# Kernel optimization log

Measured on AMD Instinct MI355X. Metric: run time of the kernel, lower is better.

Reference implementation:

```python
import jax, jax.numpy as jnp
import numpy as np
import math

B, SES, SEQ, H, K = 16, 16, 64, 512, 32
L = SES * SEQ


def setup_inputs() -> dict:
    key = jax.random.key(0)
    ks = jax.random.split(key, 16)
    s = 1.0 / math.sqrt(H)
    return {
        "user_emb": jax.random.normal(ks[0], (B, H), jnp.float32),
        "item_emb": jax.random.normal(ks[1], (B, SES, SEQ, H), jnp.float32),
        "mask": jnp.zeros((B, L, K), jnp.float32),
        "index": jax.random.randint(ks[2], (L, K), 0, L, jnp.int64),
        "Wq": jax.random.normal(ks[3], (H, H), jnp.float32) * s,
        "bq": jnp.zeros((H,), jnp.float32),
        "Wk": jax.random.normal(ks[4], (H, H), jnp.float32) * s,
        "bk": jnp.zeros((H,), jnp.float32),
        "Wv": jax.random.normal(ks[5], (H, H), jnp.float32) * s,
        "bv": jnp.zeros((H,), jnp.float32),
        "Wd": jax.random.normal(ks[6], (H, H), jnp.float32) * s,
        "bd": jnp.zeros((H,), jnp.float32),
        "ln_g": jnp.ones((H,), jnp.float32),
        "ln_b": jnp.zeros((H,), jnp.float32),
    }


def reference(user_emb, item_emb, mask, index, Wq, bq, Wk, bk, Wv, bv, Wd, bd, ln_g, ln_b):
    b, ses, seq, h = item_emb.shape
    l = ses * seq
    item_flat = item_emb.reshape(b, l, h)
    q = user_emb @ Wq.T + bq                       # [B, H]
    k = item_flat @ Wk.T + bk                      # [B, L, H]
    v = item_flat @ Wv.T + bv                      # [B, L, H]
    # scalar query against all L keys, scaled by sqrt(hidden_size)
    scores = jnp.einsum("bh,blh->bl", q, k) / math.sqrt(h)
    scores = scores[:, index] + mask               # gather -> [B, L, K]
    w = jax.nn.softmax(scores, axis=-1)            # [B, L, K]
    vg = v[:, index, :]                            # gather -> [B, L, K, H]
    attn_out = jnp.einsum("blk,blkh->blh", w, vg)  # [B, L, H]
    dense = attn_out @ Wd.T + bd
    x = dense + item_flat                          # residual (dropout = identity, eval)
    mu = jnp.mean(x, axis=-1, keepdims=True)
    var = jnp.var(x, axis=-1, keepdims=True)
    y = (x - mu) / jnp.sqrt(var + 1e-12) * ln_g + ln_b
    return y.reshape(b, ses, seq, h)
```

## Files before the change

### kernel.cpp

```cpp
#include <hip/hip_runtime.h>
#include <math.h>

constexpr int HD   = 512;
constexpr int LL   = 1024;
constexpr int MT   = 16384;
constexpr int KNBR = 32;
constexpr float SCL = 0.04419417382415922f;

typedef __attribute__((ext_vector_type(8))) short  bf16x8;
typedef __attribute__((ext_vector_type(4))) float  f32x4;

__device__ inline float b2f(unsigned short u) {
    union { unsigned int i; float f; } v; v.i = (unsigned int)u << 16; return v.f;
}
__device__ inline float b2f_lo(unsigned int u) {
    union { unsigned int i; float f; } v; v.i = u << 16; return v.f;
}
__device__ inline float b2f_hi(unsigned int u) {
    union { unsigned int i; float f; } v; v.i = u & 0xffff0000u; return v.f;
}
__device__ inline unsigned short f2b(float x) {
    union { float f; unsigned int u; } v; v.f = x;
    unsigned int r = v.u + 0x7fff + ((v.u >> 16) & 1);
    return (unsigned short)(r >> 16);
}

constexpr int PB_CONV_I = 8192;
constexpr int PB_CONV_W = 512;
constexpr int PB_Q      = 2048;

__global__ __launch_bounds__(256) void prep(
    const float* __restrict__ item, const float* __restrict__ Wv,
    const float* __restrict__ Wd, const float* __restrict__ u,
    const float* __restrict__ Wq, const float* __restrict__ bq,
    unsigned short* __restrict__ item_bf, unsigned short* __restrict__ item_kt,
    unsigned short* __restrict__ Wv_bf, unsigned short* __restrict__ Wd_bf,
    float* __restrict__ q)
{
    const int blk = blockIdx.x, tid = threadIdx.x;

    if (blk < PB_CONV_I) {
        const int i = blk * 1024 + tid * 4;
        float4 v = *(const float4*)&item[i];
        ushort4 o;
        o.x = f2b(v.x); o.y = f2b(v.y); o.z = f2b(v.z); o.w = f2b(v.w);
        *(ushort4*)&item_bf[i] = o;
        const int m = i >> 9, k = i & 511;
        *(ushort4*)&item_kt[((size_t)(k >> 5) * MT + m) * 32 + (k & 31)] = o;
        return;
    }
    if (blk < PB_CONV_I + PB_CONV_W) {
        const int n = HD*HD;
        const int i = (blk - PB_CONV_I) * 1024 + tid * 4;
        const float* s; unsigned short* d; int off;
        if (i < n) { s = Wv; d = Wv_bf; off = i; }
        else       { s = Wd; d = Wd_bf; off = i - n; }
        float4 v = *(const float4*)&s[off];
        ushort4 o;
        o.x = f2b(v.x); o.y = f2b(v.y); o.z = f2b(v.z); o.w = f2b(v.w);
        const int nr = off >> 9, k = off & 511;
        *(ushort4*)&d[((k >> 5) * 512 + nr) * 32 + (k & 31)] = o;
        return;
    }
    {
        const int wid  = (blk - PB_CONV_I - PB_CONV_W) * 4 + (tid >> 6);
        const int lane = tid & 63;
        const int b = wid >> 9, h = wid & 511;
        const float* ur = &u[b*HD + lane*8];
        const float* wr = &Wq[(size_t)h*HD + lane*8];
        const float4 u0 = *(const float4*)ur, u1 = *(const float4*)(ur+4);
        const float4 w0 = *(const float4*)wr, w1 = *(const float4*)(wr+4);
        float acc = u0.x*w0.x + u0.y*w0.y + u0.z*w0.z + u0.w*w0.w
                  + u1.x*w1.x + u1.y*w1.y + u1.z*w1.z + u1.w*w1.w;
        #pragma unroll
        for (int off = 32; off; off >>= 1) acc += __shfl_down(acc, off);
        if (lane == 0) q[b*HD + h] = acc + bq[h];
    }
}

__global__ __launch_bounds__(256) void gemm_v_r(
    const unsigned short* __restrict__ Akt, const unsigned short* __restrict__ Wt,
    const float* __restrict__ bv, const float* __restrict__ Wk,
    const float* __restrict__ bk, const float* __restrict__ q,
    unsigned short* __restrict__ v_bf, float* __restrict__ rbuf,
    float* __restrict__ s0buf)
{
    __shared__ unsigned short As[2][128 * 32];
    __shared__ unsigned short Bs[2][128 * 32];

    const int blk = blockIdx.x;
    const int tid = threadIdx.x;

    if (blk >= 512) {
        if (blk < 640) {
            __shared__ float red[4][64];
            const int rblk = blk - 512;
            const int b = rblk >> 3, c0 = (rblk & 7) * 64;
            const int cl = tid & 63, hg = tid >> 6;
            const float* qb = &q[b*HD];
            const float* wb = &Wk[(size_t)hg*128*HD + c0 + cl];
            float acc = 0.f;
            #pragma unroll 8
            for (int h = 0; h < 128; h++)
                acc += qb[hg*128 + h] * wb[(size_t)h*HD];
            red[hg][cl] = acc;
            __syncthreads();
            if (tid < 64)
                rbuf[b*HD + c0 + tid] = SCL *
                    (red[0][tid] + red[1][tid] + red[2][tid] + red[3][tid]);
        } else {
            __shared__ float sp[4];
            const int b = blk - 640;
            float p = q[b*HD + tid]*bk[tid] + q[b*HD + tid + 256]*bk[tid + 256];
            #pragma unroll
            for (int off = 32; off; off >>= 1) p += __shfl_down(p, off);
            if ((tid & 63) == 0) sp[tid >> 6] = p;
            __syncthreads();
            if (tid == 0) s0buf[b] = (sp[0] + sp[1] + sp[2] + sp[3]) * SCL;
        }
        return;
    }

    const int rowb = (blk & 7) | ((blk >> 5) << 3);
    const int colb = (blk >> 3) & 3;
    const int row0 = rowb * 128;
    const int col0 = colb * 128;

    const int wave = tid >> 6, lane = tid & 63;
    const int wm = (wave >> 1) * 64;
    const int wn = (wave & 1)  * 64;

    const int lrr = lane >> 2;
    const int cc  = lane & 3;
    int st_row[2], st_gchunk[2];
    #pragma unroll
    for (int t = 0; t < 2; t++) {
        const int m = wave*32 + t*16 + lrr;
        st_row[t]    = m;
        st_gchunk[t] = cc ^ ((m >> 1) & 3);
    }

    const int fr   = lane & 15;
    const int quad = lane >> 4;

    f32x4 acc[4][4];
    #pragma unroll
    for (int i = 0; i < 4; i++)
        #pragma unroll
        for (int j = 0; j < 4; j++)
            acc[i][j] = (f32x4){0.f, 0.f, 0.f, 0.f};

    int a_off[4], b_off[4];
    #pragma unroll
    for (int i = 0; i < 4; i++) {
        const int m = wm + i*16 + fr;
        a_off[i] = m*32 + ((quad ^ ((m >> 1) & 3)) << 3);
        const int n = wn + i*16 + fr;
        b_off[i] = n*32 + ((quad ^ ((n >> 1) & 3)) << 3);
    }

    auto stage = [&](int bf, int kt) {
        #pragma unroll
        for (int t = 0; t < 2; t++) {
            const int m = st_row[t];
            const unsigned short* ga =
                &Akt[((size_t)kt*MT + row0 + m)*32 + st_gchunk[t]*8];
            __builtin_amdgcn_global_load_lds(
                (const __attribute__((address_space(1))) void*)ga,
                (__attribute__((address_space(3))) void*)&As[bf][(wave*32 + t*16)*32],
                16, 0, 0);
            const unsigned short* gw =
                &Wt[((size_t)kt*512 + col0 + m)*32 + st_gchunk[t]*8];
            __builtin_amdgcn_global_load_lds(
                (const __attribute__((address_space(1))) void*)gw,
                (__attribute__((address_space(3))) void*)&Bs[bf][(wave*32 + t*16)*32],
                16, 0, 0);
        }
    };

    stage(0, 0);
    stage(1, 1);

    for (int s = 0; s < 15; ++s) {
        asm volatile("s_waitcnt vmcnt(4)" ::: "memory");
        __builtin_amdgcn_s_barrier();
        asm volatile("" ::: "memory");

        const int cur = s & 1;
        bf16x8 af[4], bfr[4];
        #pragma unroll
        for (int i = 0; i < 4; i++) {
            af[i]  = *(const bf16x8*)&As[cur][a_off[i]];
            bfr[i] = *(const bf16x8*)&Bs[cur][b_off[i]];
        }
        asm volatile("s_waitcnt lgkmcnt(0)" ::: "memory");
        __builtin_amdgcn_sched_barrier(0);
        __builtin_amdgcn_s_barrier();

        if (s + 2 < 16) stage(cur, s + 2);

        __builtin_amdgcn_s_setprio(1);
        #pragma unroll
        for (int i = 0; i < 4; i++)
            #pragma unroll
            for (int j = 0; j < 4; j++)
                acc[i][j] = __builtin_amdgcn_mfma_f32_16x16x32_bf16(
                    af[i], bfr[j], acc[i][j], 0, 0, 0);
        __builtin_amdgcn_s_setprio(0);
    }
    {
        asm volatile("s_waitcnt vmcnt(0)" ::: "memory");
        __builtin_amdgcn_s_barrier();
        asm volatile("" ::: "memory");
        bf16x8 af[4], bfr[4];
        #pragma unroll
        for (int i = 0; i < 4; i++) {
            af[i]  = *(const bf16x8*)&As[1][a_off[i]];
            bfr[i] = *(const bf16x8*)&Bs[1][b_off[i]];
        }
        asm volatile("s_waitcnt lgkmcnt(0)" ::: "memory");
        __builtin_amdgcn_sched_barrier(0);
        #pragma unroll
        for (int i = 0; i < 4; i++)
            #pragma unroll
            for (int j = 0; j < 4; j++)
                acc[i][j] = __builtin_amdgcn_mfma_f32_16x16x32_bf16(
                    af[i], bfr[j], acc[i][j], 0, 0, 0);
    }

    #pragma unroll
    for (int j = 0; j < 4; j++) {
        const int col = col0 + wn + j*16 + fr;
        const float bb = bv[col];
        #pragma unroll
        for (int i = 0; i < 4; i++) {
            #pragma unroll
            for (int r = 0; r < 4; r++) {
                const int row = row0 + wm + i*16 + quad*4 + r;
                v_bf[(size_t)row*HD + col] = f2b(acc[i][j][r] + bb);
            }
        }
    }
}

__global__ __launch_bounds__(256) void gp_scores(
    const float* __restrict__ rbuf, const float* __restrict__ s0buf,
    const unsigned short* __restrict__ item_bf, float* __restrict__ scores)
{
    const int m = blockIdx.x * 4 + (threadIdx.x >> 6);
    const int lane = threadIdx.x & 63;
    const int b = m >> 10;
    const unsigned short* ir = &item_bf[(size_t)m*HD + lane*8];
    const uint4 iv = *(const uint4*)ir;
    const float* rr = &rbuf[b*HD + lane*8];
    const float4 r0 = *(const float4*)rr;
    const float4 r1 = *(const float4*)(rr + 4);
    float acc = r0.x*b2f_lo(iv.x) + r0.y*b2f_hi(iv.x)
              + r0.z*b2f_lo(iv.y) + r0.w*b2f_hi(iv.y)
              + r1.x*b2f_lo(iv.z) + r1.y*b2f_hi(iv.z)
              + r1.z*b2f_lo(iv.w) + r1.w*b2f_hi(iv.w);
    #pragma unroll
    for (int off = 32; off; off >>= 1) acc += __shfl_down(acc, off);
    if (lane == 0) scores[m] = acc + s0buf[b];
}

__global__ __launch_bounds__(256) void gp_attn(
    const float* __restrict__ scores, const int* __restrict__ index,
    const float* __restrict__ mask, const unsigned short* __restrict__ v,
    unsigned short* __restrict__ attn)
{
    const int bid = blockIdx.x;
    const int m = ((bid & 7) << 11) | ((bid >> 3) << 2) | (int)(threadIdx.x >> 6);
    const int lane = threadIdx.x & 63;
    const int b = m >> 10, l = m & 1023;

    const int t = lane & 31;
    const int idx = index[l*KNBR + t];
    const float s = scores[b*LL + idx] + mask[(size_t)m*KNBR + t];

    float mx = s;
    #pragma unroll
    for (int off = 16; off; off >>= 1) mx = fmaxf(mx, __shfl_xor(mx, off));
    const float e = __expf(s - mx);
    float sum = e;
    #pragma unroll
    for (int off = 16; off; off >>= 1) sum += __shfl_xor(sum, off);
    const float w = e / sum;

    const unsigned short* vb = v + (size_t)(b << 10) * HD;
    const int loff = lane * 8;
    float a[8] = {};
    #pragma unroll 8
    for (int t2 = 0; t2 < KNBR; t2++) {
        const int   it = __builtin_amdgcn_readlane(idx, t2);
        const float wt = __int_as_float(
            __builtin_amdgcn_readlane(__float_as_int(w), t2));
        const uint4 pv = *(const uint4*)(vb + (size_t)it*HD + loff);
        a[0] += wt * b2f_lo(pv.x); a[1] += wt * b2f_hi(pv.x);
        a[2] += wt * b2f_lo(pv.y); a[3] += wt * b2f_hi(pv.y);
        a[4] += wt * b2f_lo(pv.z); a[5] += wt * b2f_hi(pv.z);
        a[6] += wt * b2f_lo(pv.w); a[7] += wt * b2f_hi(pv.w);
    }
    uint4 o;
    o.x = (unsigned int)f2b(a[0]) | ((unsigned int)f2b(a[1]) << 16);
    o.y = (unsigned int)f2b(a[2]) | ((unsigned int)f2b(a[3]) << 16);
    o.z = (unsigned int)f2b(a[4]) | ((unsigned int)f2b(a[5]) << 16);
    o.w = (unsigned int)f2b(a[6]) | ((unsigned int)f2b(a[7]) << 16);
    *(uint4*)&attn[(size_t)m*HD + lane*8] = o;
}

__global__ __launch_bounds__(256) void dense_ln(
    const unsigned short* __restrict__ A,
    const unsigned short* __restrict__ Wt,
    const float* __restrict__ bd, const unsigned short* __restrict__ res,
    const float* __restrict__ ln_g, const float* __restrict__ ln_b,
    float* __restrict__ out)
{
    __shared__ unsigned short As[2][32 * 32];
    __shared__ unsigned short Bs[2][512 * 32];
    __shared__ float rsum[4][32], rsq[4][32];

    const int tid  = threadIdx.x;
    const int wave = tid >> 6, lane = tid & 63;
    const int row0 = blockIdx.x * 32;

    const int lrr = lane >> 2;
    const int cc  = lane & 3;
    const int fr   = lane & 15;
    const int quad = lane >> 4;

    f32x4 acc[2][8];
    #pragma unroll
    for (int i = 0; i < 2; i++)
        #pragma unroll
        for (int j = 0; j < 8; j++)
            acc[i][j] = (f32x4){0.f, 0.f, 0.f, 0.f};

    int a_off[2], b_off[8];
    #pragma unroll
    for (int i = 0; i < 2; i++) {
        const int m = i*16 + fr;
        a_off[i] = m*32 + ((quad ^ ((m >> 1) & 3)) << 3);
    }
    #pragma unroll
    for (int j = 0; j < 8; j++) {
        const int n = wave*128 + j*16 + fr;
        b_off[j] = n*32 + ((quad ^ ((n >> 1) & 3)) << 3);
    }

    auto stage = [&](int bf, int kt) {
        #pragma unroll
        for (int t = 0; t < 8; t++) {
            const int n   = wave*128 + t*16 + lrr;
            const int gch = cc ^ ((n >> 1) & 3);
            const unsigned short* gw = &Wt[((size_t)kt*512 + n)*32 + gch*8];
            __builtin_amdgcn_global_load_lds(
                (const __attribute__((address_space(1))) void*)gw,
                (__attribute__((address_space(3))) void*)&Bs[bf][(wave*128 + t*16)*32],
                16, 0, 0);
        }
        if (wave < 2) {
            const int mm  = wave*16 + lrr;
            const int gch = cc ^ ((mm >> 1) & 3);
            const unsigned short* ga = &A[(size_t)(row0 + mm)*HD + kt*32 + gch*8];
            __builtin_amdgcn_global_load_lds(
                (const __attribute__((address_space(1))) void*)ga,
                (__attribute__((address_space(3))) void*)&As[bf][(wave*16)*32],
                16, 0, 0);
        }
    };

    stage(0, 0);
    stage(1, 1);

    for (int s = 0; s < 15; ++s) {
        if (wave < 2) asm volatile("s_waitcnt vmcnt(9)" ::: "memory");
        else          asm volatile("s_waitcnt vmcnt(8)" ::: "memory");
        __builtin_amdgcn_s_barrier();
        asm volatile("" ::: "memory");

        const int cur = s & 1;
        bf16x8 af[2], bfr[8];
        #pragma unroll
        for (int i = 0; i < 2; i++) af[i] = *(const bf16x8*)&As[cur][a_off[i]];
        #pragma unroll
        for (int j = 0; j < 8; j++) bfr[j] = *(const bf16x8*)&Bs[cur][b_off[j]];
        asm volatile("s_waitcnt lgkmcnt(0)" ::: "memory");
        __builtin_amdgcn_sched_barrier(0);
        __builtin_amdgcn_s_barrier();

        if (s + 2 < 16) stage(cur, s + 2);

        __builtin_amdgcn_s_setprio(1);
        #pragma unroll
        for (int i = 0; i < 2; i++)
            #pragma unroll
            for (int j = 0; j < 8; j++)
                acc[i][j] = __builtin_amdgcn_mfma_f32_16x16x32_bf16(
                    af[i], bfr[j], acc[i][j], 0, 0, 0);
        __builtin_amdgcn_s_setprio(0);
    }
    {
        asm volatile("s_waitcnt vmcnt(0)" ::: "memory");
        __builtin_amdgcn_s_barrier();
        asm volatile("" ::: "memory");
        bf16x8 af[2], bfr[8];
        #pragma unroll
        for (int i = 0; i < 2; i++) af[i] = *(const bf16x8*)&As[1][a_off[i]];
        #pragma unroll
        for (int j = 0; j < 8; j++) bfr[j] = *(const bf16x8*)&Bs[1][b_off[j]];
        asm volatile("s_waitcnt lgkmcnt(0)" ::: "memory");
        __builtin_amdgcn_sched_barrier(0);
        #pragma unroll
        for (int i = 0; i < 2; i++)
            #pragma unroll
            for (int j = 0; j < 8; j++)
                acc[i][j] = __builtin_amdgcn_mfma_f32_16x16x32_bf16(
                    af[i], bfr[j], acc[i][j], 0, 0, 0);
    }
    __syncthreads();

    unsigned short* rs = (unsigned short*)Bs;
    #pragma unroll
    for (int u = 0; u < 8; u++) {
        const int id = tid*8 + u;
        const int rr = id >> 6, c8 = id & 63;
        *(uint4*)&rs[rr*528 + c8*8] =
            *(const uint4*)&res[(size_t)(row0 + rr)*HD + c8*8];
    }
    __syncthreads();

    float bdv[8], gv[8], lbv[8];
    #pragma unroll
    for (int j = 0; j < 8; j++) {
        const int col = wave*128 + j*16 + fr;
        bdv[j] = bd[col]; gv[j] = ln_g[col]; lbv[j] = ln_b[col];
    }

    #pragma unroll
    for (int i = 0; i < 2; i++) {
        #pragma unroll
        for (int r = 0; r < 4; r++) {
            const int lrow = i*16 + quad*4 + r;
            float a1 = 0.f, a2 = 0.f;
            #pragma unroll
            for (int j = 0; j < 8; j++) {
                const int col = wave*128 + j*16 + fr;
                float val = acc[i][j][r] + bdv[j] + b2f(rs[lrow*528 + col]);
                acc[i][j][r] = val;
                a1 += val; a2 += val*val;
            }
            #pragma unroll
            for (int off = 1; off < 16; off <<= 1) {
                a1 += __shfl_xor(a1, off);
                a2 += __shfl_xor(a2, off);
            }
            if (fr == 0) { rsum[wave][lrow] = a1; rsq[wave][lrow] = a2; }
        }
    }
    __syncthreads();

    #pragma unroll
    for (int i = 0; i < 2; i++) {
        #pragma unroll
        for (int r = 0; r < 4; r++) {
            const int lrow = i*16 + quad*4 + r;
            const float tot  = rsum[0][lrow] + rsum[1][lrow] + rsum[2][lrow] + rsum[3][lrow];
            const float tot2 = rsq[0][lrow]  + rsq[1][lrow]  + rsq[2][lrow]  + rsq[3][lrow];
            const float mu  = tot * (1.f/HD);
            const float var = tot2 * (1.f/HD) - mu*mu;
            const float inv = rsqrtf(var + 1e-12f);
            const size_t gr = (size_t)(row0 + lrow) * HD;
            #pragma unroll
            for (int j = 0; j < 8; j++) {
                const int col = wave*128 + j*16 + fr;
                out[gr + col] = (acc[i][j][r] - mu)*inv*gv[j] + lbv[j];
            }
        }
    }
}

extern "C" void kernel_launch(void* const* d_in, const int* in_sizes, int n_in,
                              void* d_out, int out_size, void* d_ws, size_t ws_size,
                              hipStream_t stream) {
    const float* user_emb = (const float*)d_in[0];
    const float* item_emb = (const float*)d_in[1];
    const float* mask     = (const float*)d_in[2];
    const int*   index    = (const int*)  d_in[3];
    const float* Wq = (const float*)d_in[4];  const float* bq = (const float*)d_in[5];
    const float* Wk = (const float*)d_in[6];  const float* bk = (const float*)d_in[7];
    const float* Wv = (const float*)d_in[8];  const float* bv = (const float*)d_in[9];
    const float* Wd = (const float*)d_in[10]; const float* bd = (const float*)d_in[11];
    const float* ln_g = (const float*)d_in[12];
    const float* ln_b = (const float*)d_in[13];

    float* out = (float*)d_out;

    char* p = (char*)d_ws;
    unsigned short* item_bf = (unsigned short*)p; p += (size_t)MT*HD*2;
    unsigned short* item_kt = (unsigned short*)p; p += (size_t)MT*HD*2;
    unsigned short* v_bf    = (unsigned short*)p; p += (size_t)MT*HD*2;
    unsigned short* attn_bf = (unsigned short*)p; p += (size_t)MT*HD*2;
    unsigned short* Wv_bf   = (unsigned short*)p; p += (size_t)HD*HD*2;
    unsigned short* Wd_bf   = (unsigned short*)p; p += (size_t)HD*HD*2;
    float* q      = (float*)p; p += 16*HD*4;
    float* rbuf   = (float*)p; p += 16*HD*4;
    float* s0buf  = (float*)p; p += 16*4;
    float* scores = (float*)p; p += MT*4;

    prep<<<PB_CONV_I + PB_CONV_W + PB_Q, 256, 0, stream>>>(
        item_emb, Wv, Wd, user_emb, Wq, bq,
        item_bf, item_kt, Wv_bf, Wd_bf, q);

    gemm_v_r<<<656, 256, 0, stream>>>(item_kt, Wv_bf, bv, Wk, bk, q,
                                      v_bf, rbuf, s0buf);

    gp_scores<<<MT/4, 256, 0, stream>>>(rbuf, s0buf, item_bf, scores);

    gp_attn<<<MT/4, 256, 0, stream>>>(scores, index, mask, v_bf, attn_bf);

    dense_ln<<<MT/32, 256, 0, stream>>>(attn_bf, Wd_bf, bd, item_bf,
                                        ln_g, ln_b, out);
}
```

Measured before the change: 178.5 us.

## Fuse neighbour attention into dense+LayerNorm kernel and deepen V-GEMM pipeline

```diff
diff --git a/kernel.cpp b/kernel.cpp
--- a/kernel.cpp
+++ b/kernel.cpp
@@ -85,8 +85,8 @@
     unsigned short* __restrict__ v_bf, float* __restrict__ rbuf,
     float* __restrict__ s0buf)
 {
-    __shared__ unsigned short As[2][128 * 32];
-    __shared__ unsigned short Bs[2][128 * 32];
+    __shared__ unsigned short As[4][128 * 32];
+    __shared__ unsigned short Bs[4][128 * 32];
 
     const int blk = blockIdx.x;
     const int tid = threadIdx.x;
@@ -159,7 +159,8 @@
         b_off[i] = n*32 + ((quad ^ ((n >> 1) & 3)) << 3);
     }
 
-    auto stage = [&](int bf, int kt) {
+    auto stage = [&](int kt) {
+        const int bf = kt & 3;
         #pragma unroll
         for (int t = 0; t < 2; t++) {
             const int m = st_row[t];
@@ -178,15 +179,9 @@
         }
     };
 
-    stage(0, 0);
-    stage(1, 1);
-
-    for (int s = 0; s < 15; ++s) {
-        asm volatile("s_waitcnt vmcnt(4)" ::: "memory");
+    auto kstep = [&](int cur, int kt_next) {
         __builtin_amdgcn_s_barrier();
         asm volatile("" ::: "memory");
-
-        const int cur = s & 1;
         bf16x8 af[4], bfr[4];
         #pragma unroll
         for (int i = 0; i < 4; i++) {
@@ -196,9 +191,7 @@
         asm volatile("s_waitcnt lgkmcnt(0)" ::: "memory");
         __builtin_amdgcn_sched_barrier(0);
         __builtin_amdgcn_s_barrier();
-
-        if (s + 2 < 16) stage(cur, s + 2);
-
+        if (kt_next >= 0) stage(kt_next);
         __builtin_amdgcn_s_setprio(1);
         #pragma unroll
         for (int i = 0; i < 4; i++)
@@ -207,26 +200,17 @@
                 acc[i][j] = __builtin_amdgcn_mfma_f32_16x16x32_bf16(
                     af[i], bfr[j], acc[i][j], 0, 0, 0);
         __builtin_amdgcn_s_setprio(0);
-    }
-    {
-        asm volatile("s_waitcnt vmcnt(0)" ::: "memory");
-        __builtin_amdgcn_s_barrier();
-        asm volatile("" ::: "memory");
-        bf16x8 af[4], bfr[4];
-        #pragma unroll
-        for (int i = 0; i < 4; i++) {
-            af[i]  = *(const bf16x8*)&As[1][a_off[i]];
-            bfr[i] = *(const bf16x8*)&Bs[1][b_off[i]];
-        }
-        asm volatile("s_waitcnt lgkmcnt(0)" ::: "memory");
-        __builtin_amdgcn_sched_barrier(0);
-        #pragma unroll
-        for (int i = 0; i < 4; i++)
-            #pragma unroll
-            for (int j = 0; j < 4; j++)
-                acc[i][j] = __builtin_amdgcn_mfma_f32_16x16x32_bf16(
-                    af[i], bfr[j], acc[i][j], 0, 0, 0);
-    }
+    };
+
+    stage(0); stage(1); stage(2); stage(3);
+
+    for (int s = 0; s <= 12; ++s) {
+        asm volatile("s_waitcnt vmcnt(12)" ::: "memory");
+        kstep(s & 3, (s + 4 <= 15) ? s + 4 : -1);
+    }
+    asm volatile("s_waitcnt vmcnt(8)" ::: "memory");  kstep(1, -1);
+    asm volatile("s_waitcnt vmcnt(4)" ::: "memory");  kstep(2, -1);
+    asm volatile("s_waitcnt vmcnt(0)" ::: "memory");  kstep(3, -1);
 
     #pragma unroll
     for (int j = 0; j < 4; j++) {
@@ -264,133 +248,124 @@
     if (lane == 0) scores[m] = acc + s0buf[b];
 }
 
-__global__ __launch_bounds__(256) void gp_attn(
+__global__ __launch_bounds__(512) void dense_attn_ln(
     const float* __restrict__ scores, const int* __restrict__ index,
     const float* __restrict__ mask, const unsigned short* __restrict__ v,
-    unsigned short* __restrict__ attn)
-{
-    const int bid = blockIdx.x;
-    const int m = ((bid & 7) << 11) | ((bid >> 3) << 2) | (int)(threadIdx.x >> 6);
-    const int lane = threadIdx.x & 63;
-    const int b = m >> 10, l = m & 1023;
-
-    const int t = lane & 31;
-    const int idx = index[l*KNBR + t];
-    const float s = scores[b*LL + idx] + mask[(size_t)m*KNBR + t];
-
-    float mx = s;
-    #pragma unroll
-    for (int off = 16; off; off >>= 1) mx = fmaxf(mx, __shfl_xor(mx, off));
-    const float e = __expf(s - mx);
-    float sum = e;
-    #pragma unroll
-    for (int off = 16; off; off >>= 1) sum += __shfl_xor(sum, off);
-    const float w = e / sum;
-
-    const unsigned short* vb = v + (size_t)(b << 10) * HD;
-    const int loff = lane * 8;
-    float a[8] = {};
-    #pragma unroll 8
-    for (int t2 = 0; t2 < KNBR; t2++) {
-        const int   it = __builtin_amdgcn_readlane(idx, t2);
-        const float wt = __int_as_float(
-            __builtin_amdgcn_readlane(__float_as_int(w), t2));
-        const uint4 pv = *(const uint4*)(vb + (size_t)it*HD + loff);
-        a[0] += wt * b2f_lo(pv.x); a[1] += wt * b2f_hi(pv.x);
-        a[2] += wt * b2f_lo(pv.y); a[3] += wt * b2f_hi(pv.y);
-        a[4] += wt * b2f_lo(pv.z); a[5] += wt * b2f_hi(pv.z);
-        a[6] += wt * b2f_lo(pv.w); a[7] += wt * b2f_hi(pv.w);
-    }
-    uint4 o;
-    o.x = (unsigned int)f2b(a[0]) | ((unsigned int)f2b(a[1]) << 16);
-    o.y = (unsigned int)f2b(a[2]) | ((unsigned int)f2b(a[3]) << 16);
-    o.z = (unsigned int)f2b(a[4]) | ((unsigned int)f2b(a[5]) << 16);
-    o.w = (unsigned int)f2b(a[6]) | ((unsigned int)f2b(a[7]) << 16);
-    *(uint4*)&attn[(size_t)m*HD + lane*8] = o;
-}
-
-__global__ __launch_bounds__(256) void dense_ln(
-    const unsigned short* __restrict__ A,
     const unsigned short* __restrict__ Wt,
     const float* __restrict__ bd, const unsigned short* __restrict__ res,
     const float* __restrict__ ln_g, const float* __restrict__ ln_b,
     float* __restrict__ out)
 {
-    __shared__ unsigned short As[2][32 * 32];
     __shared__ unsigned short Bs[2][512 * 32];
-    __shared__ float rsum[4][32], rsq[4][32];
+    __shared__ unsigned short att[64 * 520];
+    __shared__ float rsum[8][64], rsq[8][64];
 
     const int tid  = threadIdx.x;
     const int wave = tid >> 6, lane = tid & 63;
-    const int row0 = blockIdx.x * 32;
-
-    const int lrr = lane >> 2;
-    const int cc  = lane & 3;
-    const int fr   = lane & 15;
-    const int quad = lane >> 4;
-
-    f32x4 acc[2][8];
-    #pragma unroll
-    for (int i = 0; i < 2; i++)
-        #pragma unroll
-        for (int j = 0; j < 8; j++)
-            acc[i][j] = (f32x4){0.f, 0.f, 0.f, 0.f};
-
-    int a_off[2], b_off[8];
-    #pragma unroll
-    for (int i = 0; i < 2; i++) {
-        const int m = i*16 + fr;
-        a_off[i] = m*32 + ((quad ^ ((m >> 1) & 3)) << 3);
-    }
-    #pragma unroll
-    for (int j = 0; j < 8; j++) {
-        const int n = wave*128 + j*16 + fr;
-        b_off[j] = n*32 + ((quad ^ ((n >> 1) & 3)) << 3);
-    }
-
-    auto stage = [&](int bf, int kt) {
-        #pragma unroll
-        for (int t = 0; t < 8; t++) {
-            const int n   = wave*128 + t*16 + lrr;
+    const int bid  = blockIdx.x;
+    const int rblk = (bid & 7) * 32 + (bid >> 3);
+    const int row0 = rblk * 64;
+    const int b    = row0 >> 10;
+
+    const int lrr = lane >> 2, cc = lane & 3;
+
+    auto stageW = [&](int bf, int kt) {
+        #pragma unroll
+        for (int t = 0; t < 4; t++) {
+            const int n   = wave*64 + t*16 + lrr;
             const int gch = cc ^ ((n >> 1) & 3);
             const unsigned short* gw = &Wt[((size_t)kt*512 + n)*32 + gch*8];
             __builtin_amdgcn_global_load_lds(
                 (const __attribute__((address_space(1))) void*)gw,
-                (__attribute__((address_space(3))) void*)&Bs[bf][(wave*128 + t*16)*32],
+                (__attribute__((address_space(3))) void*)&Bs[bf][(wave*64 + t*16)*32],
                 16, 0, 0);
         }
-        if (wave < 2) {
-            const int mm  = wave*16 + lrr;
-            const int gch = cc ^ ((mm >> 1) & 3);
-            const unsigned short* ga = &A[(size_t)(row0 + mm)*HD + kt*32 + gch*8];
-            __builtin_amdgcn_global_load_lds(
-                (const __attribute__((address_space(1))) void*)ga,
-                (__attribute__((address_space(3))) void*)&As[bf][(wave*16)*32],
-                16, 0, 0);
-        }
     };
 
-    stage(0, 0);
-    stage(1, 1);
-
-    for (int s = 0; s < 15; ++s) {
-        if (wave < 2) asm volatile("s_waitcnt vmcnt(9)" ::: "memory");
-        else          asm volatile("s_waitcnt vmcnt(8)" ::: "memory");
+    stageW(0, 0);
+    stageW(1, 1);
+
+    {
+        const unsigned short* vb = v + (size_t)b * LL * HD;
+        const int loff = lane * 8;
+        const int t = lane & 31;
+        for (int rr = 0; rr < 8; ++rr) {
+            const int lrow = wave * 8 + rr;
+            const int m = row0 + lrow;
+            const int l = m & 1023;
+
+            const int idx = index[l*KNBR + t];
+            const float s = scores[b*LL + idx] + mask[(size_t)m*KNBR + t];
+
+            float mx = s;
+            #pragma unroll
+            for (int off = 16; off; off >>= 1) mx = fmaxf(mx, __shfl_xor(mx, off));
+            const float e = __expf(s - mx);
+            float sum = e;
+            #pragma unroll
+            for (int off = 16; off; off >>= 1) sum += __shfl_xor(sum, off);
+            const float w = e / sum;
+
+            float a[8] = {};
+            #pragma unroll 8
+            for (int t2 = 0; t2 < KNBR; t2++) {
+                const int   it = __builtin_amdgcn_readlane(idx, t2);
+                const float wt = __int_as_float(
+                    __builtin_amdgcn_readlane(__float_as_int(w), t2));
+                const uint4 pv = *(const uint4*)(vb + (size_t)it*HD + loff);
+                a[0] += wt * b2f_lo(pv.x); a[1] += wt * b2f_hi(pv.x);
+                a[2] += wt * b2f_lo(pv.y); a[3] += wt * b2f_hi(pv.y);
+                a[4] += wt * b2f_lo(pv.z); a[5] += wt * b2f_hi(pv.z);
+                a[6] += wt * b2f_lo(pv.w); a[7] += wt * b2f_hi(pv.w);
+            }
+            uint4 o;
+            o.x = (unsigned int)f2b(a[0]) | ((unsigned int)f2b(a[1]) << 16);
+            o.y = (unsigned int)f2b(a[2]) | ((unsigned int)f2b(a[3]) << 16);
+            o.z = (unsigned int)f2b(a[4]) | ((unsigned int)f2b(a[5]) << 16);
+            o.w = (unsigned int)f2b(a[6]) | ((unsigned int)f2b(a[7]) << 16);
+            const int byteoff = lrow*1040 + ((lane*16) ^ ((lrow & 7) << 4));
+            *(uint4*)((char*)att + byteoff) = o;
+        }
+    }
+    asm volatile("s_waitcnt lgkmcnt(0)" ::: "memory");
+    __builtin_amdgcn_s_barrier();
+    asm volatile("" ::: "memory");
+
+    const int fr = lane & 15, quad = lane >> 4;
+    const int wr = wave >> 2, wc = wave & 3;
+
+    f32x4 acc[2][8];
+    #pragma unroll
+    for (int i = 0; i < 2; i++)
+        #pragma unroll
+        for (int j = 0; j < 8; j++)
+            acc[i][j] = (f32x4){0.f, 0.f, 0.f, 0.f};
+
+    int b_off[8];
+    #pragma unroll
+    for (int j = 0; j < 8; j++) {
+        const int n = wc*128 + j*16 + fr;
+        b_off[j] = n*32 + ((quad ^ ((n >> 1) & 3)) << 3);
+    }
+    int a_row[2];
+    #pragma unroll
+    for (int i = 0; i < 2; i++) a_row[i] = wr*32 + i*16 + fr;
+
+    auto kstep = [&](int s, int kt_next) {
         __builtin_amdgcn_s_barrier();
         asm volatile("" ::: "memory");
-
-        const int cur = s & 1;
         bf16x8 af[2], bfr[8];
         #pragma unroll
-        for (int i = 0; i < 2; i++) af[i] = *(const bf16x8*)&As[cur][a_off[i]];
-        #pragma unroll
-        for (int j = 0; j < 8; j++) bfr[j] = *(const bf16x8*)&Bs[cur][b_off[j]];
+        for (int i = 0; i < 2; i++) {
+            const int cb = (s*64 + quad*16) ^ ((a_row[i] & 7) << 4);
+            af[i] = *(const bf16x8*)((const char*)att + a_row[i]*1040 + cb);
+        }
+        #pragma unroll
+        for (int j = 0; j < 8; j++) bfr[j] = *(const bf16x8*)&Bs[s & 1][b_off[j]];
         asm volatile("s_waitcnt lgkmcnt(0)" ::: "memory");
         __builtin_amdgcn_sched_barrier(0);
         __builtin_amdgcn_s_barrier();
-
-        if (s + 2 < 16) stage(cur, s + 2);
-
+        if (kt_next >= 0) stageW(s & 1, kt_next);
         __builtin_amdgcn_s_setprio(1);
         #pragma unroll
         for (int i = 0; i < 2; i++)
@@ -399,33 +374,22 @@
                 acc[i][j] = __builtin_amdgcn_mfma_f32_16x16x32_bf16(
                     af[i], bfr[j], acc[i][j], 0, 0, 0);
         __builtin_amdgcn_s_setprio(0);
-    }
-    {
-        asm volatile("s_waitcnt vmcnt(0)" ::: "memory");
-        __builtin_amdgcn_s_barrier();
-        asm volatile("" ::: "memory");
-        bf16x8 af[2], bfr[8];
-        #pragma unroll
-        for (int i = 0; i < 2; i++) af[i] = *(const bf16x8*)&As[1][a_off[i]];
-        #pragma unroll
-        for (int j = 0; j < 8; j++) bfr[j] = *(const bf16x8*)&Bs[1][b_off[j]];
-        asm volatile("s_waitcnt lgkmcnt(0)" ::: "memory");
-        __builtin_amdgcn_sched_barrier(0);
-        #pragma unroll
-        for (int i = 0; i < 2; i++)
-            #pragma unroll
-            for (int j = 0; j < 8; j++)
-                acc[i][j] = __builtin_amdgcn_mfma_f32_16x16x32_bf16(
-                    af[i], bfr[j], acc[i][j], 0, 0, 0);
-    }
+    };
+
+    for (int s = 0; s < 15; ++s) {
+        asm volatile("s_waitcnt vmcnt(4)" ::: "memory");
+        kstep(s, (s + 2 < 16) ? s + 2 : -1);
+    }
+    asm volatile("s_waitcnt vmcnt(0)" ::: "memory");
+    kstep(15, -1);
     __syncthreads();
 
     unsigned short* rs = (unsigned short*)Bs;
     #pragma unroll
-    for (int u = 0; u < 8; u++) {
-        const int id = tid*8 + u;
+    for (int u2 = 0; u2 < 8; u2++) {
+        const int id = tid*8 + u2;
         const int rr = id >> 6, c8 = id & 63;
-        *(uint4*)&rs[rr*528 + c8*8] =
+        *(uint4*)&rs[rr*512 + c8*8] =
             *(const uint4*)&res[(size_t)(row0 + rr)*HD + c8*8];
     }
     __syncthreads();
@@ -433,7 +397,7 @@
     float bdv[8], gv[8], lbv[8];
     #pragma unroll
     for (int j = 0; j < 8; j++) {
-        const int col = wave*128 + j*16 + fr;
+        const int col = wc*128 + j*16 + fr;
         bdv[j] = bd[col]; gv[j] = ln_g[col]; lbv[j] = ln_b[col];
     }
 
@@ -441,12 +405,12 @@
     for (int i = 0; i < 2; i++) {
         #pragma unroll
         for (int r = 0; r < 4; r++) {
-            const int lrow = i*16 + quad*4 + r;
+            const int lrow = wr*32 + i*16 + quad*4 + r;
             float a1 = 0.f, a2 = 0.f;
             #pragma unroll
             for (int j = 0; j < 8; j++) {
-                const int col = wave*128 + j*16 + fr;
-                float val = acc[i][j][r] + bdv[j] + b2f(rs[lrow*528 + col]);
+                const int col = wc*128 + j*16 + fr;
+                float val = acc[i][j][r] + bdv[j] + b2f(rs[lrow*512 + col]);
                 acc[i][j][r] = val;
                 a1 += val; a2 += val*val;
             }
@@ -464,16 +428,19 @@
     for (int i = 0; i < 2; i++) {
         #pragma unroll
         for (int r = 0; r < 4; r++) {
-            const int lrow = i*16 + quad*4 + r;
-            const float tot  = rsum[0][lrow] + rsum[1][lrow] + rsum[2][lrow] + rsum[3][lrow];
-            const float tot2 = rsq[0][lrow]  + rsq[1][lrow]  + rsq[2][lrow]  + rsq[3][lrow];
+            const int lrow = wr*32 + i*16 + quad*4 + r;
+            const int wb0 = wr*4;
+            const float tot  = rsum[wb0][lrow] + rsum[wb0+1][lrow]
+                             + rsum[wb0+2][lrow] + rsum[wb0+3][lrow];
+            const float tot2 = rsq[wb0][lrow]  + rsq[wb0+1][lrow]
+                             + rsq[wb0+2][lrow]  + rsq[wb0+3][lrow];
             const float mu  = tot * (1.f/HD);
             const float var = tot2 * (1.f/HD) - mu*mu;
             const float inv = rsqrtf(var + 1e-12f);
             const size_t gr = (size_t)(row0 + lrow) * HD;
             #pragma unroll
             for (int j = 0; j < 8; j++) {
-                const int col = wave*128 + j*16 + fr;
+                const int col = wc*128 + j*16 + fr;
                 out[gr + col] = (acc[i][j][r] - mu)*inv*gv[j] + lbv[j];
             }
         }
@@ -500,7 +467,6 @@
     unsigned short* item_bf = (unsigned short*)p; p += (size_t)MT*HD*2;
     unsigned short* item_kt = (unsigned short*)p; p += (size_t)MT*HD*2;
     unsigned short* v_bf    = (unsigned short*)p; p += (size_t)MT*HD*2;
-    unsigned short* attn_bf = (unsigned short*)p; p += (size_t)MT*HD*2;
     unsigned short* Wv_bf   = (unsigned short*)p; p += (size_t)HD*HD*2;
     unsigned short* Wd_bf   = (unsigned short*)p; p += (size_t)HD*HD*2;
     float* q      = (float*)p; p += 16*HD*4;
@@ -517,8 +483,7 @@
 
     gp_scores<<<MT/4, 256, 0, stream>>>(rbuf, s0buf, item_bf, scores);
 
-    gp_attn<<<MT/4, 256, 0, stream>>>(scores, index, mask, v_bf, attn_bf);
-
-    dense_ln<<<MT/32, 256, 0, stream>>>(attn_bf, Wd_bf, bd, item_bf,
-                                        ln_g, ln_b, out);
-}
+    dense_attn_ln<<<256, 512, 0, stream>>>(scores, index, mask, v_bf,
+                                           Wd_bf, bd, item_bf,
+                                           ln_g, ln_b, out);
+}
```

New measurement: 190.5 us. +6.7%, slower.
